# Kernel tuning notes

Measured on AMD Instinct MI355X. Metric: run time of the kernel, lower is better.

## Reference

```python
import jax, jax.numpy as jnp
import numpy as np


def setup_inputs() -> dict:
    key = jax.random.key(0)
    ks = jax.random.split(key, 8)
    B, C, H, W = 8, 256, 64, 64
    inter = max(1, C // 8)  # inter_dim = in_dim // 8
    sc = 1.0 / np.sqrt(C)   # ~ conv kaiming-uniform scale
    return {
        "x": jax.random.normal(ks[0], (B, C, H, W), jnp.float32),
        "Wq": jax.random.normal(ks[1], (inter, C), jnp.float32) * sc,
        "bq": jax.random.normal(ks[2], (inter,), jnp.float32) * sc,
        "Wk": jax.random.normal(ks[3], (inter, C), jnp.float32) * sc,
        "bk": jax.random.normal(ks[4], (inter,), jnp.float32) * sc,
        "Wv": jax.random.normal(ks[5], (C, C), jnp.float32) * sc,
        "bv": jax.random.normal(ks[6], (C,), jnp.float32) * sc,
        # gamma is nn.Parameter(torch.zeros(1)); use small nonzero so the
        # attention branch actually contributes to the output.
        "gamma": jax.random.normal(ks[7], (1,), jnp.float32) * 0.1,
    }


def reference(x, Wq, bq, Wk, bk, Wv, bv, gamma):
    B, C, H, W = x.shape
    N = H * W
    xf = x.reshape(B, C, N)                                  # flatten spatial
    # 1x1 convs == per-pixel linear projections
    q = jnp.einsum('ic,bcn->bin', Wq, xf) + bq[None, :, None]  # [B, inter, N]
    k = jnp.einsum('ic,bcn->bin', Wk, xf) + bk[None, :, None]  # [B, inter, N]
    v = jnp.einsum('oc,bcn->bon', Wv, xf) + bv[None, :, None]  # [B, C, N]
    # energy[b,n,m] = sum_i q[b,i,n] * k[b,i,m]  (unscaled, non-causal)
    energy = jnp.einsum('bin,bim->bnm', q, k)                # [B, N, N]
    attention = jax.nn.softmax(energy, axis=-1)
    # attn_output[b,c,m] = sum_n attention[b,m,n] * v[b,c,n]
    attn_output = jnp.einsum('bmn,bcn->bcm', attention, v).reshape(B, C, H, W)
    return gamma[0] * attn_output + x
```

## Files before the change

kernel.cpp:

```cpp
#include <hip/hip_runtime.h>
#include <hip/hip_bf16.h>

#define BB 8
#define CC 256
#define NN 4096
#define II 32

typedef __bf16 bf16_t;
typedef bf16_t bf16x8 __attribute__((ext_vector_type(8)));
typedef float f32x4 __attribute__((ext_vector_type(4)));

__global__ __launch_bounds__(256) void wconv(
    const float* __restrict__ Wq, const float* __restrict__ Wk,
    const float* __restrict__ Wv, bf16_t* __restrict__ Wb) {
  int idx = blockIdx.x * 256 + threadIdx.x;
  int o = idx >> 8, c = idx & 255;
  float w = (o < 32) ? Wq[o * 256 + c]
          : (o < 64) ? Wk[(o - 32) * 256 + c]
                     : Wv[(o - 64) * 256 + c];
  Wb[idx] = (bf16_t)w;
}

__global__ __launch_bounds__(256, 2) void qkv_fused(
    const float* __restrict__ x, const bf16_t* __restrict__ Wb,
    const float* __restrict__ bq, const float* __restrict__ bk,
    const float* __restrict__ bv,
    bf16_t* __restrict__ q, bf16_t* __restrict__ k, bf16_t* __restrict__ v) {
  __shared__ bf16_t xs[128][264];

  const int t  = threadIdx.x;
  const int n0 = blockIdx.x * 128;
  const int og = blockIdx.y;
  const int b  = blockIdx.z;

  {
    const float* xb = x + (size_t)b * CC * NN + n0;
    const int cq  = t >> 2;
    const int nq4 = (t & 3) * 4;
#pragma unroll
    for (int p = 0; p < 8; ++p) {
      const int nb = p * 16 + nq4;
      float4 r0 = *(const float4*)&xb[(size_t)(cq * 4 + 0) * NN + nb];
      float4 r1 = *(const float4*)&xb[(size_t)(cq * 4 + 1) * NN + nb];
      float4 r2 = *(const float4*)&xb[(size_t)(cq * 4 + 2) * NN + nb];
      float4 r3 = *(const float4*)&xb[(size_t)(cq * 4 + 3) * NN + nb];
      float c0[4] = {r0.x, r0.y, r0.z, r0.w};
      float c1[4] = {r1.x, r1.y, r1.z, r1.w};
      float c2[4] = {r2.x, r2.y, r2.z, r2.w};
      float c3[4] = {r3.x, r3.y, r3.z, r3.w};
#pragma unroll
      for (int jj = 0; jj < 4; ++jj) {
        union { bf16_t h[4]; uint2 u; } pk;
        pk.h[0] = (bf16_t)c0[jj]; pk.h[1] = (bf16_t)c1[jj];
        pk.h[2] = (bf16_t)c2[jj]; pk.h[3] = (bf16_t)c3[jj];
        *(uint2*)&xs[nb + jj][cq * 4] = pk.u;
      }
    }
  }
  __syncthreads();

  const int w  = t >> 6;
  const int l  = t & 63;
  const int lo = l & 15;
  const int q4 = l >> 4;
  const int nbase = n0 + w * 32;

  f32x4 acc[10][2];
#pragma unroll
  for (int ot = 0; ot < 10; ++ot)
#pragma unroll
    for (int ms = 0; ms < 2; ++ms) acc[ot][ms] = (f32x4){0.f, 0.f, 0.f, 0.f};

#pragma unroll 2
  for (int ks = 0; ks < 8; ++ks) {
    const int c0 = ks * 32 + q4 * 8;
    bf16x8 af[2];
#pragma unroll
    for (int ms = 0; ms < 2; ++ms)
      af[ms] = *(const bf16x8*)&xs[w * 32 + ms * 16 + lo][c0];
    bf16x8 bw[10];
#pragma unroll
    for (int ot = 0; ot < 10; ++ot)
      bw[ot] = *(const bf16x8*)&Wb[((og * 10 + ot) * 16 + lo) * 256 + c0];
#pragma unroll
    for (int ms = 0; ms < 2; ++ms)
#pragma unroll
      for (int ot = 0; ot < 10; ++ot)
        acc[ot][ms] = __builtin_amdgcn_mfma_f32_16x16x32_bf16(
            af[ms], bw[ot], acc[ot][ms], 0, 0, 0);
  }

#pragma unroll
  for (int ot = 0; ot < 10; ++ot) {
    const int gt = og * 10 + ot;
    if (gt < 4) {
      const bool isq = gt < 2;
      const int i = (gt & 1) * 16 + lo;
      const float bias = isq ? bq[i] : bk[i];
      bf16_t* dst = (isq ? q : k) + (size_t)b * NN * II;
#pragma unroll
      for (int ms = 0; ms < 2; ++ms) {
#pragma unroll
        for (int r = 0; r < 4; ++r) {
          int n = nbase + ms * 16 + q4 * 4 + r;
          dst[(size_t)n * II + i] = (bf16_t)(acc[ot][ms][r] + bias);
        }
      }
    } else {
      const int ctg = gt - 4;
      const float bias = bv[ctg * 16 + lo];
      bf16_t* dst = v + (size_t)b * CC * NN;
#pragma unroll
      for (int ms = 0; ms < 2; ++ms) {
        union { bf16_t h[4]; uint2 u; } pk;
#pragma unroll
        for (int r = 0; r < 4; ++r) pk.h[r] = (bf16_t)(acc[ot][ms][r] + bias);
        const size_t idx =
            (((size_t)ctg * 512 + (nbase >> 3) + ms * 2 + (q4 >> 1)) * 16 + lo) * 8
            + (q4 & 1) * 4;
        *(uint2*)&dst[idx] = pk.u;
      }
    }
  }
}

__global__ __launch_bounds__(256, 2) void attn_mfma(
    const bf16_t* __restrict__ q, const bf16_t* __restrict__ k,
    const bf16_t* __restrict__ v, const float* __restrict__ x,
    const float* __restrict__ gamma, float* __restrict__ out) {
  __shared__ bf16_t Pld[2][64 * 64];
  __shared__ float lred[16][64];
  __shared__ float lfin[64];

  const int t  = threadIdx.x;
  const int w  = t >> 6;
  const int l  = t & 63;
  const int lo = l & 15;
  const int q4 = l >> 4;
  const int bid = blockIdx.x;
  const int b   = bid & 7;
  const int m0  = (bid >> 3) * 64;

  const bf16_t* qb = q + (size_t)b * NN * II;
  const bf16_t* kb = k + (size_t)b * NN * II;
  const bf16_t* vb = v + (size_t)b * CC * NN;

  bf16x8 qf[4];
#pragma unroll
  for (int mt = 0; mt < 4; ++mt)
    qf[mt] = *(const bf16x8*)(qb + (size_t)(m0 + mt * 16 + lo) * II + q4 * 8);

  f32x4 acc[4][4];
#pragma unroll
  for (int ct = 0; ct < 4; ++ct)
#pragma unroll
    for (int mt = 0; mt < 4; ++mt) acc[ct][mt] = (f32x4){0.f, 0.f, 0.f, 0.f};
  float lp[4] = {0.f, 0.f, 0.f, 0.f};

  const f32x4 zero = (f32x4){0.f, 0.f, 0.f, 0.f};

  bf16x8 kf = *(const bf16x8*)(kb + (size_t)(w * 16 + lo) * II + q4 * 8);

  for (int n1 = 0, it = 0; n1 < NN; n1 += 64, ++it) {
    bf16x8 vf[8];
#pragma unroll
    for (int kc = 0; kc < 2; ++kc)
#pragma unroll
      for (int ct = 0; ct < 4; ++ct)
        vf[kc * 4 + ct] = *(const bf16x8*)(vb +
            ((size_t)(w * 4 + ct) * 512 + (n1 >> 3) + kc * 4) * 128 + l * 8);
    const int n_next = (n1 + 64) & (NN - 1);
    bf16x8 kf_next = *(const bf16x8*)(kb + (size_t)(n_next + w * 16 + lo) * II + q4 * 8);

    bf16_t* Pb = Pld[it & 1];
#pragma unroll
    for (int mt = 0; mt < 4; ++mt) {
      f32x4 s = __builtin_amdgcn_mfma_f32_16x16x32_bf16(kf, qf[mt], zero, 0, 0, 0);
      float e0 = __expf(s[0]), e1 = __expf(s[1]), e2 = __expf(s[2]), e3 = __expf(s[3]);
      lp[mt] += (e0 + e1) + (e2 + e3);
      union { bf16_t h[4]; uint2 u2; } ph;
      ph.h[0] = (bf16_t)e0; ph.h[1] = (bf16_t)e1;
      ph.h[2] = (bf16_t)e2; ph.h[3] = (bf16_t)e3;
      int m_loc = mt * 16 + lo;
      int c8    = w * 2 + (q4 >> 1);
      int elem  = m_loc * 64 + ((c8 ^ (m_loc & 7)) * 8) + (q4 & 1) * 4;
      *(uint2*)&Pb[elem] = ph.u2;
    }

    asm volatile("s_waitcnt lgkmcnt(0)" ::: "memory");
    __builtin_amdgcn_s_barrier();
    __builtin_amdgcn_sched_barrier(0);

#pragma unroll
    for (int kc = 0; kc < 2; ++kc) {
      bf16x8 pf[4];
#pragma unroll
      for (int mt = 0; mt < 4; ++mt) {
        int m_loc = mt * 16 + lo;
        int c8    = kc * 4 + q4;
        pf[mt] = *(const bf16x8*)&Pb[m_loc * 64 + ((c8 ^ (m_loc & 7)) * 8)];
      }
      __builtin_amdgcn_s_setprio(1);
#pragma unroll
      for (int ct = 0; ct < 4; ++ct)
#pragma unroll
        for (int mt = 0; mt < 4; ++mt)
          acc[ct][mt] = __builtin_amdgcn_mfma_f32_16x16x32_bf16(
              vf[kc * 4 + ct], pf[mt], acc[ct][mt], 0, 0, 0);
      __builtin_amdgcn_s_setprio(0);
    }
    kf = kf_next;
  }

#pragma unroll
  for (int mt = 0; mt < 4; ++mt) lred[w * 4 + q4][mt * 16 + lo] = lp[mt];
  __syncthreads();
  if (t < 64) {
    float s = 0.f;
#pragma unroll
    for (int j = 0; j < 16; ++j) s += lred[j][t];
    lfin[t] = s;
  }
  __syncthreads();

  const float g = gamma[0];
  float linv[4];
#pragma unroll
  for (int mt = 0; mt < 4; ++mt) linv[mt] = 1.0f / lfin[mt * 16 + lo];

  const int cbase = w * 64;
#pragma unroll
  for (int ct = 0; ct < 4; ++ct) {
#pragma unroll
    for (int r = 0; r < 4; ++r) {
      int c = cbase + ct * 16 + q4 * 4 + r;
      const float* xrow = x + ((size_t)b * CC + c) * NN + m0;
      float* orow       = out + ((size_t)b * CC + c) * NN + m0;
#pragma unroll
      for (int mt = 0; mt < 4; ++mt) {
        int m = mt * 16 + lo;
        orow[m] = g * acc[ct][mt][r] * linv[mt] + xrow[m];
      }
    }
  }
}

extern "C" void kernel_launch(void* const* d_in, const int* in_sizes, int n_in,
                              void* d_out, int out_size, void* d_ws, size_t ws_size,
                              hipStream_t stream) {
  const float* x     = (const float*)d_in[0];
  const float* Wq    = (const float*)d_in[1];
  const float* bq    = (const float*)d_in[2];
  const float* Wk    = (const float*)d_in[3];
  const float* bk    = (const float*)d_in[4];
  const float* Wv    = (const float*)d_in[5];
  const float* bv    = (const float*)d_in[6];
  const float* gamma = (const float*)d_in[7];
  float* out = (float*)d_out;

  bf16_t* ws = (bf16_t*)d_ws;
  bf16_t* q  = ws;
  bf16_t* k  = q + (size_t)BB * NN * II;
  bf16_t* v  = k + (size_t)BB * NN * II;
  bf16_t* Wb = v + (size_t)BB * CC * NN;

  wconv<<<dim3(320), 256, 0, stream>>>(Wq, Wk, Wv, Wb);

  dim3 gp(NN / 128, 2, BB);
  qkv_fused<<<gp, 256, 0, stream>>>(x, Wb, bq, bk, bv, q, k, v);

  attn_mfma<<<dim3(512), 256, 0, stream>>>(q, k, v, x, gamma, out);
}
```

Measured before the change: 195.1 us.

## Split attention key loop across two wave groups and fold log2e into Q

The attention block grows to 512 threads. The two halves of the waves each process a different 64-key half of a 128-key step, and their output accumulators are reduced through shared memory at the end. Q weights and bias are pre-scaled by log2(e) so the softmax can use the hardware exp2 instead of __expf. The goal is more waves in flight and fewer loop iterations per block, at the cost of larger LDS use, an extra cross-wave reduction with barriers, and a launch bound of (512,4) that may constrain registers.

```diff
diff --git a/kernel.cpp b/kernel.cpp
--- a/kernel.cpp
+++ b/kernel.cpp
@@ -5,6 +5,13 @@
 #define CC 256
 #define NN 4096
 #define II 32
+#define LOG2E 1.4426950408889634f
+
+#if __has_builtin(__builtin_amdgcn_exp2f)
+#define EXP2F(x) __builtin_amdgcn_exp2f(x)
+#else
+#define EXP2F(x) exp2f(x)
+#endif
 
 typedef __bf16 bf16_t;
 typedef bf16_t bf16x8 __attribute__((ext_vector_type(8)));
@@ -15,7 +22,7 @@
     const float* __restrict__ Wv, bf16_t* __restrict__ Wb) {
   int idx = blockIdx.x * 256 + threadIdx.x;
   int o = idx >> 8, c = idx & 255;
-  float w = (o < 32) ? Wq[o * 256 + c]
+  float w = (o < 32) ? Wq[o * 256 + c] * LOG2E
           : (o < 64) ? Wk[(o - 32) * 256 + c]
                      : Wv[(o - 64) * 256 + c];
   Wb[idx] = (bf16_t)w;
@@ -96,7 +103,7 @@
     if (gt < 4) {
       const bool isq = gt < 2;
       const int i = (gt & 1) * 16 + lo;
-      const float bias = isq ? bq[i] : bk[i];
+      const float bias = isq ? bq[i] * LOG2E : bk[i];
       bf16_t* dst = (isq ? q : k) + (size_t)b * NN * II;
 #pragma unroll
       for (int ms = 0; ms < 2; ++ms) {
@@ -124,19 +131,22 @@
   }
 }
 
-__global__ __launch_bounds__(256, 2) void attn_mfma(
+__global__ __launch_bounds__(512, 4) void attn_mfma(
     const bf16_t* __restrict__ q, const bf16_t* __restrict__ k,
     const bf16_t* __restrict__ v, const float* __restrict__ x,
     const float* __restrict__ gamma, float* __restrict__ out) {
-  __shared__ bf16_t Pld[2][64 * 64];
-  __shared__ float lred[16][64];
+  __shared__ bf16_t Pld[2][64 * 128];
+  __shared__ f32x4 ored[4][4][64];
+  __shared__ float lred[32][64];
   __shared__ float lfin[64];
 
-  const int t  = threadIdx.x;
-  const int w  = t >> 6;
-  const int l  = t & 63;
-  const int lo = l & 15;
-  const int q4 = l >> 4;
+  const int t   = threadIdx.x;
+  const int w   = t >> 6;
+  const int w_c = w & 3;
+  const int w_n = w >> 2;
+  const int l   = t & 63;
+  const int lo  = l & 15;
+  const int q4  = l >> 4;
   const int bid = blockIdx.x;
   const int b   = bid & 7;
   const int m0  = (bid >> 3) * 64;
@@ -161,29 +171,31 @@
 
   bf16x8 kf = *(const bf16x8*)(kb + (size_t)(w * 16 + lo) * II + q4 * 8);
 
-  for (int n1 = 0, it = 0; n1 < NN; n1 += 64, ++it) {
+  for (int n1 = 0, it = 0; n1 < NN; n1 += 128, ++it) {
     bf16x8 vf[8];
 #pragma unroll
     for (int kc = 0; kc < 2; ++kc)
 #pragma unroll
       for (int ct = 0; ct < 4; ++ct)
         vf[kc * 4 + ct] = *(const bf16x8*)(vb +
-            ((size_t)(w * 4 + ct) * 512 + (n1 >> 3) + kc * 4) * 128 + l * 8);
-    const int n_next = (n1 + 64) & (NN - 1);
+            ((size_t)(w_c * 4 + ct) * 512 + ((n1 + w_n * 64) >> 3) + kc * 4) * 128
+            + l * 8);
+    const int n_next = (n1 + 128) & (NN - 1);
     bf16x8 kf_next = *(const bf16x8*)(kb + (size_t)(n_next + w * 16 + lo) * II + q4 * 8);
 
     bf16_t* Pb = Pld[it & 1];
 #pragma unroll
     for (int mt = 0; mt < 4; ++mt) {
       f32x4 s = __builtin_amdgcn_mfma_f32_16x16x32_bf16(kf, qf[mt], zero, 0, 0, 0);
-      float e0 = __expf(s[0]), e1 = __expf(s[1]), e2 = __expf(s[2]), e3 = __expf(s[3]);
+      float e0 = EXP2F(s[0]), e1 = EXP2F(s[1]);
+      float e2 = EXP2F(s[2]), e3 = EXP2F(s[3]);
       lp[mt] += (e0 + e1) + (e2 + e3);
       union { bf16_t h[4]; uint2 u2; } ph;
       ph.h[0] = (bf16_t)e0; ph.h[1] = (bf16_t)e1;
       ph.h[2] = (bf16_t)e2; ph.h[3] = (bf16_t)e3;
       int m_loc = mt * 16 + lo;
-      int c8    = w * 2 + (q4 >> 1);
-      int elem  = m_loc * 64 + ((c8 ^ (m_loc & 7)) * 8) + (q4 & 1) * 4;
+      int c16   = w * 2 + (q4 >> 1);
+      int elem  = m_loc * 128 + ((c16 ^ (m_loc & 15)) * 8) + (q4 & 1) * 4;
       *(uint2*)&Pb[elem] = ph.u2;
     }
 
@@ -197,8 +209,8 @@
 #pragma unroll
       for (int mt = 0; mt < 4; ++mt) {
         int m_loc = mt * 16 + lo;
-        int c8    = kc * 4 + q4;
-        pf[mt] = *(const bf16x8*)&Pb[m_loc * 64 + ((c8 ^ (m_loc & 7)) * 8)];
+        int c16   = (w_n * 2 + kc) * 4 + q4;
+        pf[mt] = *(const bf16x8*)&Pb[m_loc * 128 + ((c16 ^ (m_loc & 15)) * 8)];
       }
       __builtin_amdgcn_s_setprio(1);
 #pragma unroll
@@ -218,28 +230,43 @@
   if (t < 64) {
     float s = 0.f;
 #pragma unroll
-    for (int j = 0; j < 16; ++j) s += lred[j][t];
+    for (int j = 0; j < 32; ++j) s += lred[j][t];
     lfin[t] = s;
   }
   __syncthreads();
 
-  const float g = gamma[0];
-  float linv[4];
-#pragma unroll
-  for (int mt = 0; mt < 4; ++mt) linv[mt] = 1.0f / lfin[mt * 16 + lo];
-
-  const int cbase = w * 64;
 #pragma unroll
   for (int ct = 0; ct < 4; ++ct) {
-#pragma unroll
-    for (int r = 0; r < 4; ++r) {
-      int c = cbase + ct * 16 + q4 * 4 + r;
-      const float* xrow = x + ((size_t)b * CC + c) * NN + m0;
-      float* orow       = out + ((size_t)b * CC + c) * NN + m0;
-#pragma unroll
-      for (int mt = 0; mt < 4; ++mt) {
-        int m = mt * 16 + lo;
-        orow[m] = g * acc[ct][mt][r] * linv[mt] + xrow[m];
+    if (w_n == 1) {
+#pragma unroll
+      for (int mt = 0; mt < 4; ++mt) ored[w_c][mt][l] = acc[ct][mt];
+    }
+    __syncthreads();
+    if (w_n == 0) {
+#pragma unroll
+      for (int mt = 0; mt < 4; ++mt) acc[ct][mt] += ored[w_c][mt][l];
+    }
+    __syncthreads();
+  }
+
+  if (w_n == 0) {
+    const float g = gamma[0];
+    float linv[4];
+#pragma unroll
+    for (int mt = 0; mt < 4; ++mt) linv[mt] = 1.0f / lfin[mt * 16 + lo];
+    const int cbase = w_c * 64;
+#pragma unroll
+    for (int ct = 0; ct < 4; ++ct) {
+#pragma unroll
+      for (int r = 0; r < 4; ++r) {
+        int c = cbase + ct * 16 + q4 * 4 + r;
+        const float* xrow = x + ((size_t)b * CC + c) * NN + m0;
+        float* orow       = out + ((size_t)b * CC + c) * NN + m0;
+#pragma unroll
+        for (int mt = 0; mt < 4; ++mt) {
+          int m = mt * 16 + lo;
+          orow[m] = g * acc[ct][mt][r] * linv[mt] + xrow[m];
+        }
       }
     }
   }
@@ -269,5 +296,5 @@
   dim3 gp(NN / 128, 2, BB);
   qkv_fused<<<gp, 256, 0, stream>>>(x, Wb, bq, bk, bv, q, k, v);
 
-  attn_mfma<<<dim3(512), 256, 0, stream>>>(q, k, v, x, gamma, out);
+  attn_mfma<<<dim3(512), 512, 0, stream>>>(q, k, v, x, gamma, out);
 }
```

Result: slower. 290.4 us (+48.8%).

## Prefetch K/V one tile ahead with ping-pong registers and use exp2 softmax

Applied to the files above, without the earlier changes.

The attention loop is unrolled by two with ping-pong register sets, so the K fragment and all V fragments for the next tile are loaded while the current tile is computed. Before, only K was prefetched and V was loaded at the top of each iteration. Separately, Wq and bq are pre-scaled by log2(e) so the softmax can use the native exp2 instruction instead of __expf. The cost is higher VGPR pressure from the doubled V fragments, which could cause spills or lower occupancy under the 2-waves launch bound.

```diff
diff --git a/kernel.cpp b/kernel.cpp
--- a/kernel.cpp
+++ b/kernel.cpp
@@ -5,6 +5,13 @@
 #define CC 256
 #define NN 4096
 #define II 32
+#define LOG2E 1.4426950408889634f
+
+#if __has_builtin(__builtin_amdgcn_exp2f)
+#define EXP2F(x) __builtin_amdgcn_exp2f(x)
+#else
+#define EXP2F(x) exp2f(x)
+#endif
 
 typedef __bf16 bf16_t;
 typedef bf16_t bf16x8 __attribute__((ext_vector_type(8)));
@@ -15,7 +22,7 @@
     const float* __restrict__ Wv, bf16_t* __restrict__ Wb) {
   int idx = blockIdx.x * 256 + threadIdx.x;
   int o = idx >> 8, c = idx & 255;
-  float w = (o < 32) ? Wq[o * 256 + c]
+  float w = (o < 32) ? Wq[o * 256 + c] * LOG2E
           : (o < 64) ? Wk[(o - 32) * 256 + c]
                      : Wv[(o - 64) * 256 + c];
   Wb[idx] = (bf16_t)w;
@@ -96,7 +103,7 @@
     if (gt < 4) {
       const bool isq = gt < 2;
       const int i = (gt & 1) * 16 + lo;
-      const float bias = isq ? bq[i] : bk[i];
+      const float bias = isq ? bq[i] * LOG2E : bk[i];
       bf16_t* dst = (isq ? q : k) + (size_t)b * NN * II;
 #pragma unroll
       for (int ms = 0; ms < 2; ++ms) {
@@ -123,6 +130,58 @@
     }
   }
 }
+
+#define PREFETCH(NTILE, KF, VF)                                               \
+  {                                                                           \
+    const int nn_ = (NTILE);                                                  \
+    KF = *(const bf16x8*)(kb + (size_t)(nn_ + w * 16 + lo) * II + q4 * 8);    \
+    _Pragma("unroll")                                                         \
+    for (int kc = 0; kc < 2; ++kc)                                            \
+      _Pragma("unroll")                                                       \
+      for (int ct = 0; ct < 4; ++ct)                                          \
+        VF[kc * 4 + ct] = *(const bf16x8*)(vb +                               \
+            ((size_t)(w * 4 + ct) * 512 + (nn_ >> 3) + kc * 4) * 128 + l * 8);\
+  }
+
+#define ATTN_STEP(KF, VF, PBUF)                                               \
+  {                                                                           \
+    bf16_t* Pb = (PBUF);                                                      \
+    _Pragma("unroll")                                                         \
+    for (int mt = 0; mt < 4; ++mt) {                                          \
+      f32x4 s = __builtin_amdgcn_mfma_f32_16x16x32_bf16(KF, qf[mt], zero, 0, 0, 0); \
+      float e0 = EXP2F(s[0]), e1 = EXP2F(s[1]);                               \
+      float e2 = EXP2F(s[2]), e3 = EXP2F(s[3]);                               \
+      lp[mt] += (e0 + e1) + (e2 + e3);                                        \
+      union { bf16_t h[4]; uint2 u2; } ph;                                    \
+      ph.h[0] = (bf16_t)e0; ph.h[1] = (bf16_t)e1;                             \
+      ph.h[2] = (bf16_t)e2; ph.h[3] = (bf16_t)e3;                             \
+      int m_loc = mt * 16 + lo;                                               \
+      int c8    = w * 2 + (q4 >> 1);                                          \
+      int elem  = m_loc * 64 + ((c8 ^ (m_loc & 7)) * 8) + (q4 & 1) * 4;       \
+      *(uint2*)&Pb[elem] = ph.u2;                                             \
+    }                                                                         \
+    asm volatile("s_waitcnt lgkmcnt(0)" ::: "memory");                        \
+    __builtin_amdgcn_s_barrier();                                             \
+    __builtin_amdgcn_sched_barrier(0);                                        \
+    _Pragma("unroll")                                                         \
+    for (int kc = 0; kc < 2; ++kc) {                                          \
+      bf16x8 pf[4];                                                           \
+      _Pragma("unroll")                                                       \
+      for (int mt = 0; mt < 4; ++mt) {                                        \
+        int m_loc = mt * 16 + lo;                                             \
+        int c8    = kc * 4 + q4;                                              \
+        pf[mt] = *(const bf16x8*)&Pb[m_loc * 64 + ((c8 ^ (m_loc & 7)) * 8)];  \
+      }                                                                       \
+      __builtin_amdgcn_s_setprio(1);                                          \
+      _Pragma("unroll")                                                       \
+      for (int ct = 0; ct < 4; ++ct)                                          \
+        _Pragma("unroll")                                                     \
+        for (int mt = 0; mt < 4; ++mt)                                        \
+          acc[ct][mt] = __builtin_amdgcn_mfma_f32_16x16x32_bf16(              \
+              VF[kc * 4 + ct], pf[mt], acc[ct][mt], 0, 0, 0);                 \
+      __builtin_amdgcn_s_setprio(0);                                          \
+    }                                                                         \
+  }
 
 __global__ __launch_bounds__(256, 2) void attn_mfma(
     const bf16_t* __restrict__ q, const bf16_t* __restrict__ k,
@@ -159,57 +218,15 @@
 
   const f32x4 zero = (f32x4){0.f, 0.f, 0.f, 0.f};
 
-  bf16x8 kf = *(const bf16x8*)(kb + (size_t)(w * 16 + lo) * II + q4 * 8);
-
-  for (int n1 = 0, it = 0; n1 < NN; n1 += 64, ++it) {
-    bf16x8 vf[8];
-#pragma unroll
-    for (int kc = 0; kc < 2; ++kc)
-#pragma unroll
-      for (int ct = 0; ct < 4; ++ct)
-        vf[kc * 4 + ct] = *(const bf16x8*)(vb +
-            ((size_t)(w * 4 + ct) * 512 + (n1 >> 3) + kc * 4) * 128 + l * 8);
-    const int n_next = (n1 + 64) & (NN - 1);
-    bf16x8 kf_next = *(const bf16x8*)(kb + (size_t)(n_next + w * 16 + lo) * II + q4 * 8);
-
-    bf16_t* Pb = Pld[it & 1];
-#pragma unroll
-    for (int mt = 0; mt < 4; ++mt) {
-      f32x4 s = __builtin_amdgcn_mfma_f32_16x16x32_bf16(kf, qf[mt], zero, 0, 0, 0);
-      float e0 = __expf(s[0]), e1 = __expf(s[1]), e2 = __expf(s[2]), e3 = __expf(s[3]);
-      lp[mt] += (e0 + e1) + (e2 + e3);
-      union { bf16_t h[4]; uint2 u2; } ph;
-      ph.h[0] = (bf16_t)e0; ph.h[1] = (bf16_t)e1;
-      ph.h[2] = (bf16_t)e2; ph.h[3] = (bf16_t)e3;
-      int m_loc = mt * 16 + lo;
-      int c8    = w * 2 + (q4 >> 1);
-      int elem  = m_loc * 64 + ((c8 ^ (m_loc & 7)) * 8) + (q4 & 1) * 4;
-      *(uint2*)&Pb[elem] = ph.u2;
-    }
-
-    asm volatile("s_waitcnt lgkmcnt(0)" ::: "memory");
-    __builtin_amdgcn_s_barrier();
-    __builtin_amdgcn_sched_barrier(0);
-
-#pragma unroll
-    for (int kc = 0; kc < 2; ++kc) {
-      bf16x8 pf[4];
-#pragma unroll
-      for (int mt = 0; mt < 4; ++mt) {
-        int m_loc = mt * 16 + lo;
-        int c8    = kc * 4 + q4;
-        pf[mt] = *(const bf16x8*)&Pb[m_loc * 64 + ((c8 ^ (m_loc & 7)) * 8)];
-      }
-      __builtin_amdgcn_s_setprio(1);
-#pragma unroll
-      for (int ct = 0; ct < 4; ++ct)
-#pragma unroll
-        for (int mt = 0; mt < 4; ++mt)
-          acc[ct][mt] = __builtin_amdgcn_mfma_f32_16x16x32_bf16(
-              vf[kc * 4 + ct], pf[mt], acc[ct][mt], 0, 0, 0);
-      __builtin_amdgcn_s_setprio(0);
-    }
-    kf = kf_next;
+  bf16x8 kfA, kfB;
+  bf16x8 vfA[8], vfB[8];
+  PREFETCH(0, kfA, vfA)
+
+  for (int n1 = 0; n1 < NN; n1 += 128) {
+    PREFETCH(n1 + 64, kfB, vfB)
+    ATTN_STEP(kfA, vfA, Pld[0])
+    PREFETCH((n1 + 128) & (NN - 1), kfA, vfA)
+    ATTN_STEP(kfB, vfB, Pld[1])
   }
 
 #pragma unroll
```

Measured after the change: 192.4 us, median of 2. No clear change (-1.4%).

## Process 128 keys per iteration and fold log2e into Q for exp2

Applied to the files above, without the earlier changes.

The attention loop now handles 128 keys per iteration instead of 64. This halves the barriers per key and doubles the P tile in shared memory, and the second V fragment load is issued after the score/exp phase so it can overlap. Separately, Q weights and bias are prescaled by log2(e) so the softmax numerator uses the native exp2 instruction instead of __expf. Costs are more registers (two V fragment sets, two K fragments) and double the LDS for P, which may lower occupancy below two blocks per CU.

```diff
diff --git a/kernel.cpp b/kernel.cpp
--- a/kernel.cpp
+++ b/kernel.cpp
@@ -5,6 +5,13 @@
 #define CC 256
 #define NN 4096
 #define II 32
+#define LOG2E 1.4426950408889634f
+
+#if __has_builtin(__builtin_amdgcn_exp2f)
+#define EXP2F(x) __builtin_amdgcn_exp2f(x)
+#else
+#define EXP2F(x) exp2f(x)
+#endif
 
 typedef __bf16 bf16_t;
 typedef bf16_t bf16x8 __attribute__((ext_vector_type(8)));
@@ -15,7 +22,7 @@
     const float* __restrict__ Wv, bf16_t* __restrict__ Wb) {
   int idx = blockIdx.x * 256 + threadIdx.x;
   int o = idx >> 8, c = idx & 255;
-  float w = (o < 32) ? Wq[o * 256 + c]
+  float w = (o < 32) ? Wq[o * 256 + c] * LOG2E
           : (o < 64) ? Wk[(o - 32) * 256 + c]
                      : Wv[(o - 64) * 256 + c];
   Wb[idx] = (bf16_t)w;
@@ -96,7 +103,7 @@
     if (gt < 4) {
       const bool isq = gt < 2;
       const int i = (gt & 1) * 16 + lo;
-      const float bias = isq ? bq[i] : bk[i];
+      const float bias = isq ? bq[i] * LOG2E : bk[i];
       bf16_t* dst = (isq ? q : k) + (size_t)b * NN * II;
 #pragma unroll
       for (int ms = 0; ms < 2; ++ms) {
@@ -128,7 +135,7 @@
     const bf16_t* __restrict__ q, const bf16_t* __restrict__ k,
     const bf16_t* __restrict__ v, const float* __restrict__ x,
     const float* __restrict__ gamma, float* __restrict__ out) {
-  __shared__ bf16_t Pld[2][64 * 64];
+  __shared__ bf16_t Pld[2][64 * 128];
   __shared__ float lred[16][64];
   __shared__ float lfin[64];
 
@@ -159,57 +166,75 @@
 
   const f32x4 zero = (f32x4){0.f, 0.f, 0.f, 0.f};
 
-  bf16x8 kf = *(const bf16x8*)(kb + (size_t)(w * 16 + lo) * II + q4 * 8);
-
-  for (int n1 = 0, it = 0; n1 < NN; n1 += 64, ++it) {
-    bf16x8 vf[8];
+  bf16x8 kf0 = *(const bf16x8*)(kb + (size_t)(w * 32 + lo) * II + q4 * 8);
+  bf16x8 kf1 = *(const bf16x8*)(kb + (size_t)(w * 32 + 16 + lo) * II + q4 * 8);
+
+  for (int n1 = 0; n1 < NN; n1 += 128) {
+    bf16_t* Pb = Pld[(n1 >> 7) & 1];
+
+    bf16x8 vf0[8];
 #pragma unroll
     for (int kc = 0; kc < 2; ++kc)
 #pragma unroll
       for (int ct = 0; ct < 4; ++ct)
-        vf[kc * 4 + ct] = *(const bf16x8*)(vb +
+        vf0[kc * 4 + ct] = *(const bf16x8*)(vb +
             ((size_t)(w * 4 + ct) * 512 + (n1 >> 3) + kc * 4) * 128 + l * 8);
-    const int n_next = (n1 + 64) & (NN - 1);
-    bf16x8 kf_next = *(const bf16x8*)(kb + (size_t)(n_next + w * 16 + lo) * II + q4 * 8);
-
-    bf16_t* Pb = Pld[it & 1];
-#pragma unroll
-    for (int mt = 0; mt < 4; ++mt) {
-      f32x4 s = __builtin_amdgcn_mfma_f32_16x16x32_bf16(kf, qf[mt], zero, 0, 0, 0);
-      float e0 = __expf(s[0]), e1 = __expf(s[1]), e2 = __expf(s[2]), e3 = __expf(s[3]);
-      lp[mt] += (e0 + e1) + (e2 + e3);
-      union { bf16_t h[4]; uint2 u2; } ph;
-      ph.h[0] = (bf16_t)e0; ph.h[1] = (bf16_t)e1;
-      ph.h[2] = (bf16_t)e2; ph.h[3] = (bf16_t)e3;
-      int m_loc = mt * 16 + lo;
-      int c8    = w * 2 + (q4 >> 1);
-      int elem  = m_loc * 64 + ((c8 ^ (m_loc & 7)) * 8) + (q4 & 1) * 4;
-      *(uint2*)&Pb[elem] = ph.u2;
-    }
+
+#pragma unroll
+    for (int s = 0; s < 2; ++s) {
+      const bf16x8 kf = s ? kf1 : kf0;
+#pragma unroll
+      for (int mt = 0; mt < 4; ++mt) {
+        f32x4 sc = __builtin_amdgcn_mfma_f32_16x16x32_bf16(kf, qf[mt], zero, 0, 0, 0);
+        float e0 = EXP2F(sc[0]), e1 = EXP2F(sc[1]);
+        float e2 = EXP2F(sc[2]), e3 = EXP2F(sc[3]);
+        lp[mt] += (e0 + e1) + (e2 + e3);
+        union { bf16_t h[4]; uint2 u2; } ph;
+        ph.h[0] = (bf16_t)e0; ph.h[1] = (bf16_t)e1;
+        ph.h[2] = (bf16_t)e2; ph.h[3] = (bf16_t)e3;
+        int m_loc = mt * 16 + lo;
+        int c16   = w * 4 + s * 2 + (q4 >> 1);
+        int elem  = m_loc * 128 + ((c16 ^ (m_loc & 7)) * 8) + (q4 & 1) * 4;
+        *(uint2*)&Pb[elem] = ph.u2;
+      }
+    }
+
+    bf16x8 vf1[8];
+#pragma unroll
+    for (int kc = 0; kc < 2; ++kc)
+#pragma unroll
+      for (int ct = 0; ct < 4; ++ct)
+        vf1[kc * 4 + ct] = *(const bf16x8*)(vb +
+            ((size_t)(w * 4 + ct) * 512 + ((n1 + 64) >> 3) + kc * 4) * 128 + l * 8);
+    const int n_next = (n1 + 128) & (NN - 1);
+    bf16x8 kf0n = *(const bf16x8*)(kb + (size_t)(n_next + w * 32 + lo) * II + q4 * 8);
+    bf16x8 kf1n = *(const bf16x8*)(kb + (size_t)(n_next + w * 32 + 16 + lo) * II + q4 * 8);
 
     asm volatile("s_waitcnt lgkmcnt(0)" ::: "memory");
     __builtin_amdgcn_s_barrier();
     __builtin_amdgcn_sched_barrier(0);
 
 #pragma unroll
-    for (int kc = 0; kc < 2; ++kc) {
+    for (int kc = 0; kc < 4; ++kc) {
       bf16x8 pf[4];
 #pragma unroll
       for (int mt = 0; mt < 4; ++mt) {
         int m_loc = mt * 16 + lo;
-        int c8    = kc * 4 + q4;
-        pf[mt] = *(const bf16x8*)&Pb[m_loc * 64 + ((c8 ^ (m_loc & 7)) * 8)];
+        int c16   = kc * 4 + q4;
+        pf[mt] = *(const bf16x8*)&Pb[m_loc * 128 + ((c16 ^ (m_loc & 7)) * 8)];
       }
       __builtin_amdgcn_s_setprio(1);
 #pragma unroll
-      for (int ct = 0; ct < 4; ++ct)
+      for (int ct = 0; ct < 4; ++ct) {
+        const bf16x8 vfc = (kc < 2) ? vf0[kc * 4 + ct] : vf1[(kc - 2) * 4 + ct];
 #pragma unroll
         for (int mt = 0; mt < 4; ++mt)
           acc[ct][mt] = __builtin_amdgcn_mfma_f32_16x16x32_bf16(
-              vf[kc * 4 + ct], pf[mt], acc[ct][mt], 0, 0, 0);
+              vfc, pf[mt], acc[ct][mt], 0, 0, 0);
+      }
       __builtin_amdgcn_s_setprio(0);
     }
-    kf = kf_next;
+    kf0 = kf0n; kf1 = kf1n;
   }
 
 #pragma unroll
```

Result: no change. 193.9 us (-0.6%).
